# Kernel tuning notes

Measured on AMD Instinct MI355X. Metric: run time of the kernel, lower is better.

The kernel has to match this reference:

```python
import jax, jax.numpy as jnp
import numpy as np

B, N, DIN, DOUT, H = 4, 2048, 256, 256, 4
HD = DOUT // H
NEG_SLOPE = 0.2


def setup_inputs() -> dict:
    key = jax.random.key(0)
    k1, k2, k3, k4, k5 = jax.random.split(key, 5)
    x = jax.random.normal(k1, (B, N, DIN), dtype=jnp.float32)
    adj = jax.random.randint(k2, (B, N, N), 0, 2).astype(jnp.float32)
    # ensure self-loops so every softmax row has at least one valid entry
    adj = jnp.maximum(adj, jnp.eye(N, dtype=jnp.float32)[None])
    # xavier-uniform-ish scales
    w_bound = float(np.sqrt(6.0 / (DIN + DOUT)))
    a_bound = float(np.sqrt(6.0 / (1 + HD)))
    W = jax.random.uniform(k3, (DOUT, DIN), jnp.float32, -w_bound, w_bound)
    a_src = jax.random.uniform(k4, (H, HD), jnp.float32, -a_bound, a_bound)
    a_dst = jax.random.uniform(k5, (H, HD), jnp.float32, -a_bound, a_bound)
    return {"x": x, "adj": adj, "W": W, "a_src": a_src, "a_dst": a_dst}


def reference(x, adj, W, a_src, a_dst):
    b, n, _ = x.shape
    h = (x @ W.T).reshape(b, n, H, HD)                      # [B,N,H,HD]
    s_src = jnp.einsum('bnhd,hd->bnh', h, a_src)            # [B,N,H]
    s_dst = jnp.einsum('bnhd,hd->bnh', h, a_dst)            # [B,N,H]
    # e[b,i,j,h] = leaky_relu(s_src[b,i,h] + s_dst[b,j,h])
    e = jax.nn.leaky_relu(s_src[:, :, None, :] + s_dst[:, None, :, :], NEG_SLOPE)
    e = jnp.where(adj[..., None] == 0, -jnp.inf, e)         # [B,N,N,H]
    alpha = jax.nn.softmax(e, axis=2)                       # softmax over j (dropout is identity at eval)
    out = jnp.einsum('bijh,bjhd->bihd', alpha, h)           # weighted aggregate
    return out.reshape(b, n, DOUT)
```

## Files before the change

kernel.cpp:

```cpp
#include <hip/hip_runtime.h>
#include <math.h>

#define Bb   4
#define Nn   2048
#define Dd   256
#define Hh   4
#define HDd  64
#define BN   (Bb * Nn)

typedef float v4f __attribute__((ext_vector_type(4)));
typedef short v8s __attribute__((ext_vector_type(8)));

__device__ __forceinline__ unsigned rne_bf16(float f) {
    unsigned u = __float_as_uint(f);
    u += 0x7fffu + ((u >> 16) & 1u);
    return u >> 16;
}

__global__ __launch_bounds__(256, 2) void k_gemm(const float* __restrict__ x,
                                                 const float* __restrict__ W,
                                                 const float* __restrict__ a_src,
                                                 const float* __restrict__ a_dst,
                                                 const float* __restrict__ adj,
                                                 unsigned short* __restrict__ hbf,
                                                 float* __restrict__ ssrc,
                                                 float* __restrict__ sdst,
                                                 unsigned long long* __restrict__ bitadj) {
    __shared__ __align__(16) unsigned short xs[2][64 * 72];
    __shared__ __align__(16) unsigned short wsm[2][64 * 72];
    __shared__ float asd[128];

    const int bid0 = (int)blockIdx.x;
    if (bid0 & 1) {
        const int gw = (bid0 >> 1) * 4 + ((int)threadIdx.x >> 6);
        const int lane = (int)threadIdx.x & 63;
#pragma unroll 1
        for (int w = gw * 4; w < 262144; w += 2048 * 4) {
            float v0 = adj[(size_t)((w + 0) >> 5) * 2048 + ((w + 0) & 31) * 64 + lane];
            float v1 = adj[(size_t)((w + 1) >> 5) * 2048 + ((w + 1) & 31) * 64 + lane];
            float v2 = adj[(size_t)((w + 2) >> 5) * 2048 + ((w + 2) & 31) * 64 + lane];
            float v3 = adj[(size_t)((w + 3) >> 5) * 2048 + ((w + 3) & 31) * 64 + lane];
            unsigned long long m0 = __ballot(v0 != 0.0f);
            unsigned long long m1 = __ballot(v1 != 0.0f);
            unsigned long long m2 = __ballot(v2 != 0.0f);
            unsigned long long m3 = __ballot(v3 != 0.0f);
            if (lane == 0) {
                bitadj[w + 0] = m0;
                bitadj[w + 1] = m1;
                bitadj[w + 2] = m2;
                bitadj[w + 3] = m3;
            }
        }
        return;
    }

    const int g = bid0 >> 1;
    const int head = (g >> 2) & 3;
    const int mtile = (g & 3) + 4 * (g >> 4);
    const int tid = threadIdx.x;
    const int m0 = mtile * 64;
    const int n0 = head * 64;
    const int b = m0 >> 11;
    const int i0loc = m0 & 2047;

    if (tid < 128) {
        int sel = tid >> 6, d = tid & 63;
        asd[tid] = sel ? a_dst[n0 + d] : a_src[n0 + d];
    }

    const int wv = tid >> 6, ln = tid & 63, l15 = ln & 15, l4 = ln >> 4;
    const int mh = wv >> 1, nh = wv & 1;
    const int srow = tid >> 2, kq = (tid & 3) * 16;

    v4f acc[2][2];
#pragma unroll
    for (int gg = 0; gg < 2; ++gg)
#pragma unroll
        for (int t = 0; t < 2; ++t) acc[gg][t] = (v4f){0.f, 0.f, 0.f, 0.f};

    for (int st = 0; st < 4; ++st) {
        const int k0 = st * 64;
        __syncthreads();
        {
            float xf[16], wf[16];
            const float* xp = x + (size_t)(m0 + srow) * Dd + k0 + kq;
            const float* wp = W + (size_t)(n0 + srow) * Dd + k0 + kq;
#pragma unroll
            for (int q = 0; q < 4; ++q) {
                *(float4*)&xf[q * 4] = *(const float4*)(xp + q * 4);
                *(float4*)&wf[q * 4] = *(const float4*)(wp + q * 4);
            }
            unsigned xh[8], xl[8], wh[8], wl[8];
#pragma unroll
            for (int j = 0; j < 8; ++j) {
                unsigned h0 = rne_bf16(xf[2 * j]), h1 = rne_bf16(xf[2 * j + 1]);
                float l0 = xf[2 * j] - __uint_as_float(h0 << 16);
                float l1 = xf[2 * j + 1] - __uint_as_float(h1 << 16);
                xh[j] = h0 | (h1 << 16);
                xl[j] = rne_bf16(l0) | (rne_bf16(l1) << 16);
                unsigned g0 = rne_bf16(wf[2 * j]), g1 = rne_bf16(wf[2 * j + 1]);
                float m0f = wf[2 * j] - __uint_as_float(g0 << 16);
                float m1f = wf[2 * j + 1] - __uint_as_float(g1 << 16);
                wh[j] = g0 | (g1 << 16);
                wl[j] = rne_bf16(m0f) | (rne_bf16(m1f) << 16);
            }
            *(uint4*)(xs[0] + srow * 72 + kq)     = make_uint4(xh[0], xh[1], xh[2], xh[3]);
            *(uint4*)(xs[0] + srow * 72 + kq + 8) = make_uint4(xh[4], xh[5], xh[6], xh[7]);
            *(uint4*)(xs[1] + srow * 72 + kq)     = make_uint4(xl[0], xl[1], xl[2], xl[3]);
            *(uint4*)(xs[1] + srow * 72 + kq + 8) = make_uint4(xl[4], xl[5], xl[6], xl[7]);
            *(uint4*)(wsm[0] + srow * 72 + kq)     = make_uint4(wh[0], wh[1], wh[2], wh[3]);
            *(uint4*)(wsm[0] + srow * 72 + kq + 8) = make_uint4(wh[4], wh[5], wh[6], wh[7]);
            *(uint4*)(wsm[1] + srow * 72 + kq)     = make_uint4(wl[0], wl[1], wl[2], wl[3]);
            *(uint4*)(wsm[1] + srow * 72 + kq + 8) = make_uint4(wl[4], wl[5], wl[6], wl[7]);
        }
        __syncthreads();
        {
            v8s ah[2][2], al[2][2], bh_[2][2], bl_[2][2];
#pragma unroll
            for (int gg = 0; gg < 2; ++gg)
#pragma unroll
                for (int kh = 0; kh < 2; ++kh) {
                    int ro = (mh * 32 + gg * 16 + l15) * 72 + kh * 32 + l4 * 8;
                    ah[gg][kh] = *(const v8s*)(xs[0] + ro);
                    al[gg][kh] = *(const v8s*)(xs[1] + ro);
                }
#pragma unroll
            for (int t = 0; t < 2; ++t)
#pragma unroll
                for (int kh = 0; kh < 2; ++kh) {
                    int ro = (nh * 32 + t * 16 + l15) * 72 + kh * 32 + l4 * 8;
                    bh_[t][kh] = *(const v8s*)(wsm[0] + ro);
                    bl_[t][kh] = *(const v8s*)(wsm[1] + ro);
                }
#pragma unroll
            for (int gg = 0; gg < 2; ++gg)
#pragma unroll
                for (int t = 0; t < 2; ++t)
#pragma unroll
                    for (int kh = 0; kh < 2; ++kh) {
                        acc[gg][t] = __builtin_amdgcn_mfma_f32_16x16x32_bf16(ah[gg][kh], bh_[t][kh], acc[gg][t], 0, 0, 0);
                        acc[gg][t] = __builtin_amdgcn_mfma_f32_16x16x32_bf16(al[gg][kh], bh_[t][kh], acc[gg][t], 0, 0, 0);
                        acc[gg][t] = __builtin_amdgcn_mfma_f32_16x16x32_bf16(ah[gg][kh], bl_[t][kh], acc[gg][t], 0, 0, 0);
                    }
        }
    }

    __syncthreads();
    float* T = (float*)&xs[0][0];
#pragma unroll
    for (int gg = 0; gg < 2; ++gg)
#pragma unroll
        for (int t = 0; t < 2; ++t)
#pragma unroll
            for (int r = 0; r < 4; ++r) {
                int d = nh * 32 + t * 16 + l15;
                int m = mh * 32 + gg * 16 + l4 * 4 + r;
                T[d * 67 + m] = acc[gg][t][r];
            }
    __syncthreads();
    if (tid < 128) {
        int m = tid & 63, sel = tid >> 6;
        float s = 0.f;
#pragma unroll
        for (int d = 0; d < 64; ++d) s += T[d * 67 + m] * asd[sel * 64 + d];
        (sel ? sdst : ssrc)[(size_t)head * BN + (size_t)b * Nn + i0loc + m] = s;
        int dloc = tid >> 1, jhh = tid & 1;
        const float* row = T + dloc * 67 + jhh * 32;
        unsigned pk[16];
#pragma unroll
        for (int jj = 0; jj < 16; ++jj)
            pk[jj] = rne_bf16(row[jj * 2]) | (rne_bf16(row[jj * 2 + 1]) << 16);
        unsigned short* dst = hbf +
            ((size_t)((b * 64 + (i0loc >> 5) + jhh) * 256 + head * HDd + dloc)) * 32;
        uint4* d4 = (uint4*)dst;
        d4[0] = make_uint4(pk[0], pk[1], pk[2], pk[3]);
        d4[1] = make_uint4(pk[4], pk[5], pk[6], pk[7]);
        d4[2] = make_uint4(pk[8], pk[9], pk[10], pk[11]);
        d4[3] = make_uint4(pk[12], pk[13], pk[14], pk[15]);
    }
}

__global__ __launch_bounds__(512, 4) void k_aggr(const unsigned short* __restrict__ hbf,
                                                 const unsigned long long* __restrict__ bitadj,
                                                 const float* __restrict__ ssrc,
                                                 const float* __restrict__ sdst,
                                                 float* __restrict__ out) {
    __shared__ __align__(16) float dtab[4 * 2048 * 2];

    const int tid = threadIdx.x;
    const int bid = (int)blockIdx.x;
    const int xcd = bid & 7;
    const int b   = xcd >> 1;
    const int i0  = (((bid >> 3) << 1) | (xcd & 1)) * 16;

    const int wv = tid >> 6;
    const int h  = wv & 3;
    const int jh = wv >> 2;
    const int ln = tid & 63, l15 = ln & 15, l4 = ln >> 4;

    for (int q = tid; q < 2048; q += 512) {
        int hh = q >> 9, j4 = (q & 511) * 4;
        float4 sv = *(const float4*)(sdst + (size_t)hh * BN + (size_t)b * Nn + j4);
        float4 o0 = make_float4(__expf(sv.x), __expf(0.2f * sv.x),
                                __expf(sv.y), __expf(0.2f * sv.y));
        float4 o1 = make_float4(__expf(sv.z), __expf(0.2f * sv.z),
                                __expf(sv.w), __expf(0.2f * sv.w));
        *(float4*)&dtab[(hh * 2048 + j4) * 2]     = o0;
        *(float4*)&dtab[(hh * 2048 + j4) * 2 + 4] = o1;
    }

    const int irow = i0 + l15;
    const float ss = ssrc[(size_t)h * BN + (size_t)b * Nn + irow];
    const float c1 = __expf(ss), c2 = __expf(0.2f * ss);
    const unsigned char* ajr = (const unsigned char*)bitadj +
        ((size_t)b * Nn + irow) * 256 + jh * 128;
    const unsigned short* hb0 = hbf +
        ((size_t)b * 64 * 256 + (size_t)(h * HDd + l15)) * 32 + l4 * 8;
    const float* dtb = dtab + (h * 2048 + jh * 1024 + l4 * 8) * 2;

    const v8s ones = {0x3F80, 0x3F80, 0x3F80, 0x3F80, 0x3F80, 0x3F80, 0x3F80, 0x3F80};

    v4f acc0 = (v4f){0.f, 0.f, 0.f, 0.f}, acc1 = acc0, acc2 = acc0, acc3 = acc0, zac = acc0;
    v8s bbA[8], bbB[8];
    unsigned mA0, mB0, mA1, mB1;

    __syncthreads();

#define LOADB(S_, BB) do {                                                    \
        const unsigned short* hq_ = hb0 +                                     \
            (size_t)((jh * 16 + ((S_) & 15)) * 16384);                        \
        BB[0] = *(const v8s*)(hq_ + 0);                                       \
        BB[1] = *(const v8s*)(hq_ + 8192);                                    \
        BB[2] = *(const v8s*)(hq_ + 512);                                     \
        BB[3] = *(const v8s*)(hq_ + 8192 + 512);                              \
        BB[4] = *(const v8s*)(hq_ + 1024);                                    \
        BB[5] = *(const v8s*)(hq_ + 8192 + 1024);                             \
        BB[6] = *(const v8s*)(hq_ + 1536);                                    \
        BB[7] = *(const v8s*)(hq_ + 8192 + 1536);                             \
    } while (0)

#define LOADADJ(S_, MA_, MB_) do {                                            \
        MA_ = ajr[((S_) & 15) * 8 + l4];                                      \
        MB_ = ajr[((S_) & 15) * 8 + 4 + l4];                                  \
    } while (0)

#define GENFRAG(dst, M_, dd_) do {                                            \
        const float4 q0_ = *(const float4*)((dd_) + 0);                       \
        const float4 q1_ = *(const float4*)((dd_) + 4);                       \
        const float4 q2_ = *(const float4*)((dd_) + 8);                       \
        const float4 q3_ = *(const float4*)((dd_) + 12);                      \
        float w0_ = ((M_) & 1u)   ? fmaxf(c1 * q0_.x, c2 * q0_.y) : 0.f;      \
        float w1_ = ((M_) & 2u)   ? fmaxf(c1 * q0_.z, c2 * q0_.w) : 0.f;      \
        float w2_ = ((M_) & 4u)   ? fmaxf(c1 * q1_.x, c2 * q1_.y) : 0.f;      \
        float w3_ = ((M_) & 8u)   ? fmaxf(c1 * q1_.z, c2 * q1_.w) : 0.f;      \
        float w4_ = ((M_) & 16u)  ? fmaxf(c1 * q2_.x, c2 * q2_.y) : 0.f;      \
        float w5_ = ((M_) & 32u)  ? fmaxf(c1 * q2_.z, c2 * q2_.w) : 0.f;      \
        float w6_ = ((M_) & 64u)  ? fmaxf(c1 * q3_.x, c2 * q3_.y) : 0.f;      \
        float w7_ = ((M_) & 128u) ? fmaxf(c1 * q3_.z, c2 * q3_.w) : 0.f;      \
        union { v8s v; unsigned u[4]; } P_;                                   \
        asm("v_cvt_pk_bf16_f32 %0, %1, %2" : "=v"(P_.u[0]) : "v"(w0_), "v"(w1_)); \
        asm("v_cvt_pk_bf16_f32 %0, %1, %2" : "=v"(P_.u[1]) : "v"(w2_), "v"(w3_)); \
        asm("v_cvt_pk_bf16_f32 %0, %1, %2" : "=v"(P_.u[2]) : "v"(w4_), "v"(w5_)); \
        asm("v_cvt_pk_bf16_f32 %0, %1, %2" : "=v"(P_.u[3]) : "v"(w6_), "v"(w7_)); \
        dst = P_.v;                                                           \
    } while (0)

#define STEPX(S_, BB, MA_, MB_) do {                                          \
        const float* dd_ = dtb + (S_) * 128;                                  \
        v8s afr0_, afr1_;                                                     \
        GENFRAG(afr0_, MA_, dd_);                                             \
        GENFRAG(afr1_, MB_, dd_ + 64);                                        \
        acc0 = __builtin_amdgcn_mfma_f32_16x16x32_bf16(afr0_, BB[0], acc0, 0, 0, 0); \
        acc1 = __builtin_amdgcn_mfma_f32_16x16x32_bf16(afr0_, BB[2], acc1, 0, 0, 0); \
        acc2 = __builtin_amdgcn_mfma_f32_16x16x32_bf16(afr0_, BB[4], acc2, 0, 0, 0); \
        acc3 = __builtin_amdgcn_mfma_f32_16x16x32_bf16(afr0_, BB[6], acc3, 0, 0, 0); \
        zac  = __builtin_amdgcn_mfma_f32_16x16x32_bf16(afr0_, ones,  zac,  0, 0, 0); \
        acc0 = __builtin_amdgcn_mfma_f32_16x16x32_bf16(afr1_, BB[1], acc0, 0, 0, 0); \
        acc1 = __builtin_amdgcn_mfma_f32_16x16x32_bf16(afr1_, BB[3], acc1, 0, 0, 0); \
        acc2 = __builtin_amdgcn_mfma_f32_16x16x32_bf16(afr1_, BB[5], acc2, 0, 0, 0); \
        acc3 = __builtin_amdgcn_mfma_f32_16x16x32_bf16(afr1_, BB[7], acc3, 0, 0, 0); \
        zac  = __builtin_amdgcn_mfma_f32_16x16x32_bf16(afr1_, ones,  zac,  0, 0, 0); \
    } while (0)

    LOADB(0, bbA);
    LOADADJ(0, mA0, mB0);
#pragma unroll 1
    for (int s = 0; s < 16; s += 2) {
        LOADB(s + 1, bbB);
        LOADADJ(s + 1, mA1, mB1);
        __builtin_amdgcn_sched_barrier(0);
        STEPX(s, bbA, mA0, mB0);
        LOADB(s + 2, bbA);
        LOADADJ(s + 2, mA0, mB0);
        __builtin_amdgcn_sched_barrier(0);
        STEPX(s + 1, bbB, mA1, mB1);
    }

#undef LOADB
#undef LOADADJ
#undef GENFRAG
#undef STEPX

    __syncthreads();
    float* red = dtab;
    float* rp = red + (h * 64 + ln) * 20;
    if (jh) {
        *(v4f*)(rp + 0)  = acc0;
        *(v4f*)(rp + 4)  = acc1;
        *(v4f*)(rp + 8)  = acc2;
        *(v4f*)(rp + 12) = acc3;
        *(v4f*)(rp + 16) = zac;
    }
    __syncthreads();
    if (!jh) {
        acc0 += *(const v4f*)(rp + 0);
        acc1 += *(const v4f*)(rp + 4);
        acc2 += *(const v4f*)(rp + 8);
        acc3 += *(const v4f*)(rp + 12);
        zac  += *(const v4f*)(rp + 16);
        float zi[4];
#pragma unroll
        for (int r = 0; r < 4; ++r) zi[r] = 1.f / zac[r];
        float* op = out + ((size_t)b * Nn + i0 + l4 * 4) * Dd + h * HDd + l15;
#pragma unroll
        for (int r = 0; r < 4; ++r) {
            op[(size_t)r * Dd + 0]  = acc0[r] * zi[r];
            op[(size_t)r * Dd + 16] = acc1[r] * zi[r];
            op[(size_t)r * Dd + 32] = acc2[r] * zi[r];
            op[(size_t)r * Dd + 48] = acc3[r] * zi[r];
        }
    }
}

extern "C" void kernel_launch(void* const* d_in, const int* in_sizes, int n_in,
                              void* d_out, int out_size, void* d_ws, size_t ws_size,
                              hipStream_t stream) {
    const float* x     = (const float*)d_in[0];
    const float* adj   = (const float*)d_in[1];
    const float* W     = (const float*)d_in[2];
    const float* a_src = (const float*)d_in[3];
    const float* a_dst = (const float*)d_in[4];
    float* out = (float*)d_out;

    unsigned short* hbf = (unsigned short*)d_ws;
    float* ssrc = (float*)(hbf + (size_t)Bb * Nn * Dd);
    float* sdst = ssrc + (size_t)Hh * BN;
    unsigned long long* bitadj = (unsigned long long*)(sdst + (size_t)Hh * BN);

    k_gemm<<<dim3(1024), dim3(256), 0, stream>>>(x, W, a_src, a_dst, adj,
                                                 hbf, ssrc, sdst, bitadj);
    k_aggr<<<dim3(512), dim3(512), 0, stream>>>(hbf, bitadj, ssrc, sdst, out);
}
```

Before: 168.9 us.

## Split aggregation waves over heads, row subtiles and d-halves instead of j-halves

Reorganizes the aggregation kernel so each block covers two heads and 32 rows. Each wave handles one head, one 16-row subtile and one half of the head dimension, and walks the full j range. This removes the cross-wave j-split reduction through shared memory and halves the softmax exp table in LDS, which may raise occupancy. The trade-off is that the weight-fragment generation is now duplicated across the two d-half waves, and each wave runs a longer serial loop with fewer MFMAs per fragment.

```diff
diff --git a/kernel.cpp b/kernel.cpp
--- a/kernel.cpp
+++ b/kernel.cpp
@@ -185,22 +185,26 @@
                                                  const float* __restrict__ ssrc,
                                                  const float* __restrict__ sdst,
                                                  float* __restrict__ out) {
-    __shared__ __align__(16) float dtab[4 * 2048 * 2];
+    __shared__ __align__(16) float dtab[2 * 2048 * 2];
+    __shared__ __align__(16) float zsh[2][2][16];
 
     const int tid = threadIdx.x;
     const int bid = (int)blockIdx.x;
     const int xcd = bid & 7;
     const int b   = xcd >> 1;
-    const int i0  = (((bid >> 3) << 1) | (xcd & 1)) * 16;
-
-    const int wv = tid >> 6;
-    const int h  = wv & 3;
-    const int jh = wv >> 2;
+    const int hp  = xcd & 1;
+    const int itile = bid >> 3;
+
+    const int wv   = tid >> 6;
+    const int hloc = wv >> 2;
+    const int h    = hp * 2 + hloc;
+    const int isub = (wv >> 1) & 1;
+    const int dh   = wv & 1;
     const int ln = tid & 63, l15 = ln & 15, l4 = ln >> 4;
 
-    for (int q = tid; q < 2048; q += 512) {
+    for (int q = tid; q < 1024; q += 512) {
         int hh = q >> 9, j4 = (q & 511) * 4;
-        float4 sv = *(const float4*)(sdst + (size_t)hh * BN + (size_t)b * Nn + j4);
+        float4 sv = *(const float4*)(sdst + (size_t)(hp * 2 + hh) * BN + (size_t)b * Nn + j4);
         float4 o0 = make_float4(__expf(sv.x), __expf(0.2f * sv.x),
                                 __expf(sv.y), __expf(0.2f * sv.y));
         float4 o1 = make_float4(__expf(sv.z), __expf(0.2f * sv.z),
@@ -209,40 +213,31 @@
         *(float4*)&dtab[(hh * 2048 + j4) * 2 + 4] = o1;
     }
 
-    const int irow = i0 + l15;
+    const int irow = itile * 32 + isub * 16 + l15;
     const float ss = ssrc[(size_t)h * BN + (size_t)b * Nn + irow];
     const float c1 = __expf(ss), c2 = __expf(0.2f * ss);
     const unsigned char* ajr = (const unsigned char*)bitadj +
-        ((size_t)b * Nn + irow) * 256 + jh * 128;
+        ((size_t)b * Nn + irow) * 256;
+    const int dg0 = h * HDd + dh * 32;
     const unsigned short* hb0 = hbf +
-        ((size_t)b * 64 * 256 + (size_t)(h * HDd + l15)) * 32 + l4 * 8;
-    const float* dtb = dtab + (h * 2048 + jh * 1024 + l4 * 8) * 2;
+        ((size_t)b * 64 * 256 + (size_t)(dg0 + l15)) * 32 + l4 * 8;
+    const float* dtb = dtab + (hloc * 2048 + l4 * 8) * 2;
 
     const v8s ones = {0x3F80, 0x3F80, 0x3F80, 0x3F80, 0x3F80, 0x3F80, 0x3F80, 0x3F80};
 
-    v4f acc0 = (v4f){0.f, 0.f, 0.f, 0.f}, acc1 = acc0, acc2 = acc0, acc3 = acc0, zac = acc0;
-    v8s bbA[8], bbB[8];
-    unsigned mA0, mB0, mA1, mB1;
+    v4f acc0 = (v4f){0.f, 0.f, 0.f, 0.f}, acc1 = acc0, zac = acc0;
+    v8s b0A, b1A, b0B, b1B;
+    unsigned mA, mB;
 
     __syncthreads();
 
-#define LOADB(S_, BB) do {                                                    \
-        const unsigned short* hq_ = hb0 +                                     \
-            (size_t)((jh * 16 + ((S_) & 15)) * 16384);                        \
-        BB[0] = *(const v8s*)(hq_ + 0);                                       \
-        BB[1] = *(const v8s*)(hq_ + 8192);                                    \
-        BB[2] = *(const v8s*)(hq_ + 512);                                     \
-        BB[3] = *(const v8s*)(hq_ + 8192 + 512);                              \
-        BB[4] = *(const v8s*)(hq_ + 1024);                                    \
-        BB[5] = *(const v8s*)(hq_ + 8192 + 1024);                             \
-        BB[6] = *(const v8s*)(hq_ + 1536);                                    \
-        BB[7] = *(const v8s*)(hq_ + 8192 + 1536);                             \
+#define LOADB(JC_, B0_, B1_) do {                                             \
+        const unsigned short* hq_ = hb0 + (size_t)(JC_) * 8192;               \
+        B0_ = *(const v8s*)(hq_);                                             \
+        B1_ = *(const v8s*)(hq_ + 512);                                       \
     } while (0)
 
-#define LOADADJ(S_, MA_, MB_) do {                                            \
-        MA_ = ajr[((S_) & 15) * 8 + l4];                                      \
-        MB_ = ajr[((S_) & 15) * 8 + 4 + l4];                                  \
-    } while (0)
+#define LOADM(JC_, M_) do { M_ = ajr[(JC_) * 4 + l4]; } while (0)
 
 #define GENFRAG(dst, M_, dd_) do {                                            \
         const float4 q0_ = *(const float4*)((dd_) + 0);                       \
@@ -265,70 +260,44 @@
         dst = P_.v;                                                           \
     } while (0)
 
-#define STEPX(S_, BB, MA_, MB_) do {                                          \
-        const float* dd_ = dtb + (S_) * 128;                                  \
-        v8s afr0_, afr1_;                                                     \
-        GENFRAG(afr0_, MA_, dd_);                                             \
-        GENFRAG(afr1_, MB_, dd_ + 64);                                        \
-        acc0 = __builtin_amdgcn_mfma_f32_16x16x32_bf16(afr0_, BB[0], acc0, 0, 0, 0); \
-        acc1 = __builtin_amdgcn_mfma_f32_16x16x32_bf16(afr0_, BB[2], acc1, 0, 0, 0); \
-        acc2 = __builtin_amdgcn_mfma_f32_16x16x32_bf16(afr0_, BB[4], acc2, 0, 0, 0); \
-        acc3 = __builtin_amdgcn_mfma_f32_16x16x32_bf16(afr0_, BB[6], acc3, 0, 0, 0); \
-        zac  = __builtin_amdgcn_mfma_f32_16x16x32_bf16(afr0_, ones,  zac,  0, 0, 0); \
-        acc0 = __builtin_amdgcn_mfma_f32_16x16x32_bf16(afr1_, BB[1], acc0, 0, 0, 0); \
-        acc1 = __builtin_amdgcn_mfma_f32_16x16x32_bf16(afr1_, BB[3], acc1, 0, 0, 0); \
-        acc2 = __builtin_amdgcn_mfma_f32_16x16x32_bf16(afr1_, BB[5], acc2, 0, 0, 0); \
-        acc3 = __builtin_amdgcn_mfma_f32_16x16x32_bf16(afr1_, BB[7], acc3, 0, 0, 0); \
-        zac  = __builtin_amdgcn_mfma_f32_16x16x32_bf16(afr1_, ones,  zac,  0, 0, 0); \
+#define STEPX(JC_, M_, B0_, B1_) do {                                         \
+        const float* dd_ = dtb + (JC_) * 64;                                  \
+        v8s afr_;                                                             \
+        GENFRAG(afr_, M_, dd_);                                               \
+        acc0 = __builtin_amdgcn_mfma_f32_16x16x32_bf16(afr_, B0_, acc0, 0, 0, 0); \
+        acc1 = __builtin_amdgcn_mfma_f32_16x16x32_bf16(afr_, B1_, acc1, 0, 0, 0); \
+        zac  = __builtin_amdgcn_mfma_f32_16x16x32_bf16(afr_, ones, zac,  0, 0, 0); \
     } while (0)
 
-    LOADB(0, bbA);
-    LOADADJ(0, mA0, mB0);
+    LOADB(0, b0A, b1A);
+    LOADM(0, mA);
 #pragma unroll 1
-    for (int s = 0; s < 16; s += 2) {
-        LOADB(s + 1, bbB);
-        LOADADJ(s + 1, mA1, mB1);
+    for (int jc = 0; jc < 64; jc += 2) {
+        LOADB(jc + 1, b0B, b1B);
+        LOADM(jc + 1, mB);
         __builtin_amdgcn_sched_barrier(0);
-        STEPX(s, bbA, mA0, mB0);
-        LOADB(s + 2, bbA);
-        LOADADJ(s + 2, mA0, mB0);
+        STEPX(jc, mA, b0A, b1A);
+        LOADB((jc + 2) & 63, b0A, b1A);
+        LOADM((jc + 2) & 63, mA);
         __builtin_amdgcn_sched_barrier(0);
-        STEPX(s + 1, bbB, mA1, mB1);
+        STEPX(jc + 1, mB, b0B, b1B);
     }
 
 #undef LOADB
-#undef LOADADJ
+#undef LOADM
 #undef GENFRAG
 #undef STEPX
 
+    if (dh == 0 && l15 == 0)
+        *(v4f*)&zsh[hloc][isub][l4 * 4] = zac;
     __syncthreads();
-    float* red = dtab;
-    float* rp = red + (h * 64 + ln) * 20;
-    if (jh) {
-        *(v4f*)(rp + 0)  = acc0;
-        *(v4f*)(rp + 4)  = acc1;
-        *(v4f*)(rp + 8)  = acc2;
-        *(v4f*)(rp + 12) = acc3;
-        *(v4f*)(rp + 16) = zac;
-    }
-    __syncthreads();
-    if (!jh) {
-        acc0 += *(const v4f*)(rp + 0);
-        acc1 += *(const v4f*)(rp + 4);
-        acc2 += *(const v4f*)(rp + 8);
-        acc3 += *(const v4f*)(rp + 12);
-        zac  += *(const v4f*)(rp + 16);
-        float zi[4];
-#pragma unroll
-        for (int r = 0; r < 4; ++r) zi[r] = 1.f / zac[r];
-        float* op = out + ((size_t)b * Nn + i0 + l4 * 4) * Dd + h * HDd + l15;
-#pragma unroll
-        for (int r = 0; r < 4; ++r) {
-            op[(size_t)r * Dd + 0]  = acc0[r] * zi[r];
-            op[(size_t)r * Dd + 16] = acc1[r] * zi[r];
-            op[(size_t)r * Dd + 32] = acc2[r] * zi[r];
-            op[(size_t)r * Dd + 48] = acc3[r] * zi[r];
-        }
+    const v4f zv = *(const v4f*)&zsh[hloc][isub][l4 * 4];
+    float* op = out + ((size_t)b * Nn + itile * 32 + isub * 16 + l4 * 4) * Dd + dg0 + l15;
+#pragma unroll
+    for (int r = 0; r < 4; ++r) {
+        float zi = 1.f / zv[r];
+        op[(size_t)r * Dd + 0]  = acc0[r] * zi;
+        op[(size_t)r * Dd + 16] = acc1[r] * zi;
     }
 }
 
```

Result: slower. 175.5 us (+3.9%).
